# Kernel optimization log

Hardware: AMD Instinct MI355X
Metric: run time of the kernel (lower is better)

## Reference

```python
import jax, jax.numpy as jnp
import numpy as np

B, N, C, H = 8, 1024, 768, 12
TEMP = 0.1


def setup_inputs() -> dict:
    key = jax.random.key(0)
    k1, k2, k3 = jax.random.split(key, 3)
    x = jax.random.normal(k1, (B, N, C), dtype=jnp.float32)
    # nn.MultiheadAttention params (bias=False since qkv_bias=False)
    w_in = jax.random.normal(k2, (3 * C, C), dtype=jnp.float32) * 0.02   # in_proj_weight
    w_out = jax.random.normal(k3, (C, C), dtype=jnp.float32) * 0.02      # out_proj.weight
    sm_w = jnp.ones((3,), dtype=jnp.float32)                             # Conv1d(1,1,3) init ones
    return {"x": x, "w_in": w_in, "w_out": w_out, "sm_w": sm_w}


def reference(x, w_in, w_out, sm_w):
    Bq, Nq, Cq = x.shape
    hd = Cq // H
    # in-projection (torch Linear: y = x @ W^T)
    qkv = x @ w_in.T                                   # [B,N,3C]
    q, k, v = jnp.split(qkv, 3, axis=-1)
    to_heads = lambda t: t.reshape(Bq, Nq, H, hd).transpose(0, 2, 1, 3)  # [B,H,N,hd]
    q, k, v = to_heads(q), to_heads(k), to_heads(v)
    scale = 1.0 / np.sqrt(hd)
    logits = jnp.einsum("bhqd,bhkd->bhqk", q, k) * scale
    attn = jax.nn.softmax(logits, axis=-1)             # [B,H,N,N]
    ctx = jnp.einsum("bhqk,bhkd->bhqd", attn, v)
    ctx = ctx.transpose(0, 2, 1, 3).reshape(Bq, Nq, Cq)
    x_out = ctx @ w_out.T                              # [B,N,C]

    # average_attn_weights=True -> mean over heads
    aw = attn.mean(axis=1)                             # [B,N,N]
    # central finite difference with replicate padding along key dim
    p = jnp.pad(aw, ((0, 0), (0, 0), (1, 1)), mode="edge")
    grad = (p[:, :, 2:] - p[:, :, :-2]) * 0.5
    importance = jnp.abs(grad).sum(axis=1)             # sum over query dim -> [B,N]

    # Conv1d(1,1,k=3,pad=1,bias=False): cross-correlation with zero padding
    ip = jnp.pad(importance, ((0, 0), (1, 1)))
    sm = sm_w[0] * ip[:, :-2] + sm_w[1] * ip[:, 1:-1] + sm_w[2] * ip[:, 2:]

    # eval path: final_scores = importance_scores (no EMA)
    mu = sm.mean(axis=-1, keepdims=True)
    sd = jnp.std(sm, axis=-1, keepdims=True, ddof=1)   # torch std is unbiased
    fs = (sm - mu) / (sd + 1e-6)
    final_scores = jax.nn.softmax(fs / TEMP, axis=-1)  # [B,N]
    return x_out, final_scores
```

## Files before the change

### kernel.cpp

```cpp
#include <hip/hip_runtime.h>

#define NSEQ  1024
#define NHEAD 12
#define HDIM  64
#define CDIM  768
#define BATCH 8

typedef short bf16x8 __attribute__((ext_vector_type(8)));
typedef float f32x4  __attribute__((ext_vector_type(4)));

__device__ __forceinline__ float bf2f(unsigned short h) {
  unsigned u = ((unsigned)h) << 16;
  float f;
  __builtin_memcpy(&f, &u, 4);
  return f;
}
__device__ __forceinline__ unsigned short f2bf(float f) {
  unsigned u;
  __builtin_memcpy(&u, &f, 4);
  u = (u + 0x7fffu + ((u >> 16) & 1u)) >> 16;
  return (unsigned short)u;
}

__device__ __forceinline__ size_t qk_off(size_t bh, int s, int d) {
  return ((((bh * 64 + (s >> 4)) * 2 + (d >> 5)) * 64) + (((d >> 3) & 3) * 16) + (s & 15)) * 8 + (d & 7);
}
__device__ __forceinline__ size_t v_off(size_t bh, int key, int d) {
  return ((((bh * 4 + (d >> 4)) * 32 + (key >> 5)) * 64) + (((key >> 3) & 3) * 16) + (d & 15)) * 8 + (key & 7);
}

#define GLD16(GP, LP) __builtin_amdgcn_global_load_lds( \
    (const __attribute__((address_space(1))) void*)(GP), \
    (__attribute__((address_space(3))) void*)(LP), 16, 0, 0)

__global__ __launch_bounds__(256)
void convert_kernel(const float* __restrict__ x, const float* __restrict__ w_in,
                    const float* __restrict__ w_out,
                    unsigned short* __restrict__ xh, unsigned short* __restrict__ xl,
                    unsigned short* __restrict__ wih, unsigned short* __restrict__ wil,
                    unsigned short* __restrict__ woh)
{
  const int idx = (blockIdx.x * 256 + threadIdx.x) * 4;
  if (idx < 6291456) {
    float4 v = *(const float4*)(x + idx);
    ushort4 h, l;
    h.x = f2bf(v.x); l.x = f2bf(v.x - bf2f(h.x));
    h.y = f2bf(v.y); l.y = f2bf(v.y - bf2f(h.y));
    h.z = f2bf(v.z); l.z = f2bf(v.z - bf2f(h.z));
    h.w = f2bf(v.w); l.w = f2bf(v.w - bf2f(h.w));
    *(ushort4*)(xh + idx) = h;
    *(ushort4*)(xl + idx) = l;
  } else if (idx < 6291456 + 1769472) {
    const int j = idx - 6291456;
    float4 v = *(const float4*)(w_in + j);
    ushort4 h, l;
    h.x = f2bf(v.x); l.x = f2bf(v.x - bf2f(h.x));
    h.y = f2bf(v.y); l.y = f2bf(v.y - bf2f(h.y));
    h.z = f2bf(v.z); l.z = f2bf(v.z - bf2f(h.z));
    h.w = f2bf(v.w); l.w = f2bf(v.w - bf2f(h.w));
    *(ushort4*)(wih + j) = h;
    *(ushort4*)(wil + j) = l;
  } else {
    const int j = idx - 8060928;
    float4 v = *(const float4*)(w_out + j);
    ushort4 h;
    h.x = f2bf(v.x); h.y = f2bf(v.y); h.z = f2bf(v.z); h.w = f2bf(v.w);
    *(ushort4*)(woh + j) = h;
  }
}

template<int MODE>
__global__ __launch_bounds__(256)
void gemm_mfma(const unsigned short* __restrict__ Ah, const unsigned short* __restrict__ Al,
               const unsigned short* __restrict__ Bh, const unsigned short* __restrict__ Bl,
               float* __restrict__ Cout,
               unsigned short* __restrict__ Qfh, unsigned short* __restrict__ Qfl,
               unsigned short* __restrict__ Kfh, unsigned short* __restrict__ Kfl,
               unsigned short* __restrict__ Vf)
{
  __shared__ unsigned short Asm[128][64];
  __shared__ unsigned short Bsm[128][64];
  const int t    = threadIdx.x;
  const int lane = t & 63;
  const int wid  = t >> 6;
  const int c    = lane & 15;
  const int g    = lane >> 4;
  const int id   = blockIdx.x;
  const int xcd  = id & 7;
  const int j    = id >> 3;
  const int bm   = (j & 7) + xcd * 8;
  const int bn   = j >> 3;
  const int sec    = (MODE == 0) ? (bn / 6) : 0;
  const int nsteps = (MODE == 0 && sec < 2) ? 36 : 12;

  f32x4 acc[4][4];
#pragma unroll
  for (int mi = 0; mi < 4; ++mi)
#pragma unroll
    for (int ni = 0; ni < 4; ++ni) acc[mi][ni] = (f32x4){0.f, 0.f, 0.f, 0.f};

  const size_t Am0 = (size_t)bm * 128;
  const size_t Bn0 = (size_t)bn * 128;
  const int srow = wid * 32 + (lane >> 3);
  const int scol = (lane & 7) * 8;
  const int mh = (wid & 1) * 64;
  const int nh = (wid >> 1) * 64;

  for (int ks = 0; ks < nsteps; ++ks) {
    const int ksec = (ks >= 24) ? 2 : ((ks >= 12) ? 1 : 0);
    const int kin  = (ks - ksec * 12) * 64;
    const unsigned short* Asrc = (ksec == 1) ? Al : Ah;
    const unsigned short* Bsrc = (ksec == 2) ? Bl : Bh;
    __syncthreads();
#pragma unroll
    for (int i = 0; i < 4; ++i) {
      GLD16(Asrc + (Am0 + srow + i * 8) * 768 + kin + scol, &Asm[wid * 32 + i * 8][0]);
      GLD16(Bsrc + (Bn0 + srow + i * 8) * 768 + kin + scol, &Bsm[wid * 32 + i * 8][0]);
    }
    __syncthreads();
#pragma unroll
    for (int kk = 0; kk < 2; ++kk) {
      bf16x8 a[4], bb[4];
#pragma unroll
      for (int mi = 0; mi < 4; ++mi)
        a[mi] = *(const bf16x8*)&Asm[mh + mi * 16 + c][kk * 32 + g * 8];
#pragma unroll
      for (int ni = 0; ni < 4; ++ni)
        bb[ni] = *(const bf16x8*)&Bsm[nh + ni * 16 + c][kk * 32 + g * 8];
#pragma unroll
      for (int mi = 0; mi < 4; ++mi)
#pragma unroll
        for (int ni = 0; ni < 4; ++ni)
          acc[mi][ni] = __builtin_amdgcn_mfma_f32_16x16x32_bf16(a[mi], bb[ni], acc[mi][ni], 0, 0, 0);
    }
  }

  if (MODE == 1) {
#pragma unroll
    for (int mi = 0; mi < 4; ++mi) {
#pragma unroll
      for (int r = 0; r < 4; ++r) {
        const int m = bm * 128 + mh + mi * 16 + g * 4 + r;
#pragma unroll
        for (int ni = 0; ni < 4; ++ni) {
          const int n = bn * 128 + nh + ni * 16 + c;
          Cout[(size_t)m * 768 + n] = acc[mi][ni][r];
        }
      }
    }
  } else {
#pragma unroll
    for (int mi = 0; mi < 4; ++mi) {
#pragma unroll
      for (int r = 0; r < 4; ++r) {
        const int m   = bm * 128 + mh + mi * 16 + g * 4 + r;
        const int bi  = m >> 10;
        const int qi  = m & 1023;
#pragma unroll
        for (int ni = 0; ni < 4; ++ni) {
          const int n  = bn * 128 + nh + ni * 16 + c;
          const int np = n - sec * 768;
          const int h  = np >> 6;
          const int d  = np & 63;
          const size_t bh = (size_t)(bi * 12 + h);
          float v = acc[mi][ni][r];
          if (sec == 0) {
            v *= 0.125f;
            size_t off = qk_off(bh, qi, d);
            unsigned short hi = f2bf(v);
            Qfh[off] = hi;
            Qfl[off] = f2bf(v - bf2f(hi));
          } else if (sec == 1) {
            size_t off = qk_off(bh, qi, d);
            unsigned short hi = f2bf(v);
            Kfh[off] = hi;
            Kfl[off] = f2bf(v - bf2f(hi));
          } else {
            Vf[v_off(bh, qi, d)] = f2bf(v);
          }
        }
      }
    }
  }
}

struct AttnSmem {
  union {
    unsigned short P[16][1032];
    float AW[8][1032];
  } u;
  float Cpart[4][16][64];
  float red[16][4];
};

__global__ __launch_bounds__(256, 2)
void attn_mfma(const unsigned short* __restrict__ Qfh, const unsigned short* __restrict__ Qfl,
               const unsigned short* __restrict__ Kfh, const unsigned short* __restrict__ Kfl,
               const unsigned short* __restrict__ Vf,
               unsigned short* __restrict__ CtxG, float* __restrict__ Imp)
{
  __shared__ AttnSmem sm;
  const int t    = threadIdx.x;
  const int lane = t & 63;
  const int wid  = t >> 6;
  const int g    = lane >> 4;
  const int c    = lane & 15;
  const int b    = blockIdx.x & 7;
  const int qt   = blockIdx.x >> 3;
  const int q0   = qt * 16;

  float aw[16][4];
#pragma unroll
  for (int kt = 0; kt < 16; ++kt)
#pragma unroll
    for (int r = 0; r < 4; ++r) aw[kt][r] = 0.f;

  for (int h = 0; h < 12; ++h) {
    const size_t bh = (size_t)b * 12 + h;

    const size_t qbase = ((bh * 64 + qt) * 2) * 512 + lane * 8;
    bf16x8 qh0 = *(const bf16x8*)(Qfh + qbase);
    bf16x8 qh1 = *(const bf16x8*)(Qfh + qbase + 512);
    bf16x8 ql0 = *(const bf16x8*)(Qfl + qbase);
    bf16x8 ql1 = *(const bf16x8*)(Qfl + qbase + 512);

    f32x4 acc[16];
#pragma unroll
    for (int kt = 0; kt < 16; ++kt) acc[kt] = (f32x4){0.f, 0.f, 0.f, 0.f};
    const size_t kbase = ((bh * 64 + wid * 16) * 2) * 512 + lane * 8;
#pragma unroll
    for (int kt = 0; kt < 16; ++kt) {
      const size_t kb = kbase + (size_t)kt * 1024;
      bf16x8 kh0 = *(const bf16x8*)(Kfh + kb);
      bf16x8 kh1 = *(const bf16x8*)(Kfh + kb + 512);
      bf16x8 kl0 = *(const bf16x8*)(Kfl + kb);
      bf16x8 kl1 = *(const bf16x8*)(Kfl + kb + 512);
      f32x4 a = acc[kt];
      a = __builtin_amdgcn_mfma_f32_16x16x32_bf16(qh0, kh0, a, 0, 0, 0);
      a = __builtin_amdgcn_mfma_f32_16x16x32_bf16(qh1, kh1, a, 0, 0, 0);
      a = __builtin_amdgcn_mfma_f32_16x16x32_bf16(qh0, kl0, a, 0, 0, 0);
      a = __builtin_amdgcn_mfma_f32_16x16x32_bf16(qh1, kl1, a, 0, 0, 0);
      a = __builtin_amdgcn_mfma_f32_16x16x32_bf16(ql0, kh0, a, 0, 0, 0);
      a = __builtin_amdgcn_mfma_f32_16x16x32_bf16(ql1, kh1, a, 0, 0, 0);
      acc[kt] = a;
    }

    float sume[4];
#pragma unroll
    for (int r = 0; r < 4; ++r) {
      float s = 0.f;
#pragma unroll
      for (int kt = 0; kt < 16; ++kt) {
        float e = __expf(fminf(acc[kt][r], 80.f));
        acc[kt][r] = e;
        s += e;
      }
      s += __shfl_xor(s, 1);
      s += __shfl_xor(s, 2);
      s += __shfl_xor(s, 4);
      s += __shfl_xor(s, 8);
      sume[r] = s;
    }
    if (c == 0) {
#pragma unroll
      for (int r = 0; r < 4; ++r) sm.red[g * 4 + r][wid] = sume[r];
    }
    __syncthreads();
#pragma unroll
    for (int r = 0; r < 4; ++r) {
      const float* rp = sm.red[g * 4 + r];
      float inv = 1.f / ((rp[0] + rp[1]) + (rp[2] + rp[3]));
#pragma unroll
      for (int kt = 0; kt < 16; ++kt) {
        float p = acc[kt][r] * inv;
        aw[kt][r] += p * (1.f / 12.f);
        sm.u.P[g * 4 + r][wid * 256 + kt * 16 + c] = f2bf(p);
      }
    }

    f32x4 cacc[4];
#pragma unroll
    for (int dt = 0; dt < 4; ++dt) cacc[dt] = (f32x4){0.f, 0.f, 0.f, 0.f};
    const size_t vbase = (bh * 4) * 32 * 512 + (size_t)wid * 8 * 512 + lane * 8;
#pragma unroll
    for (int ks = 0; ks < 8; ++ks) {
      bf16x8 pf = *(const bf16x8*)&sm.u.P[c][wid * 256 + ks * 32 + g * 8];
#pragma unroll
      for (int dt = 0; dt < 4; ++dt) {
        bf16x8 vf = *(const bf16x8*)(Vf + vbase + ((size_t)dt * 32 + ks) * 512);
        cacc[dt] = __builtin_amdgcn_mfma_f32_16x16x32_bf16(pf, vf, cacc[dt], 0, 0, 0);
      }
    }
#pragma unroll
    for (int dt = 0; dt < 4; ++dt)
#pragma unroll
      for (int r = 0; r < 4; ++r)
        sm.Cpart[wid][g * 4 + r][dt * 16 + c] = cacc[dt][r];
    __syncthreads();
    for (int i = t; i < 1024; i += 256) {
      int qi = i >> 6, d = i & 63;
      float s = (sm.Cpart[0][qi][d] + sm.Cpart[1][qi][d]) +
                (sm.Cpart[2][qi][d] + sm.Cpart[3][qi][d]);
      CtxG[((size_t)(b * 1024 + q0 + qi)) * 768 + h * 64 + d] = f2bf(s);
    }
    __syncthreads();
  }

  float ia[4] = {0.f, 0.f, 0.f, 0.f};
#pragma unroll
  for (int half = 0; half < 2; ++half) {
    if ((g >> 1) == half) {
#pragma unroll
      for (int kt = 0; kt < 16; ++kt)
#pragma unroll
        for (int r = 0; r < 4; ++r)
          sm.u.AW[(g & 1) * 4 + r][wid * 256 + kt * 16 + c] = aw[kt][r];
    }
    __syncthreads();
#pragma unroll
    for (int qi = 0; qi < 8; ++qi) {
#pragma unroll
      for (int cc = 0; cc < 4; ++cc) {
        int k = t * 4 + cc;
        float am = sm.u.AW[qi][k == 0 ? 0 : k - 1];
        float ap = sm.u.AW[qi][k == 1023 ? 1023 : k + 1];
        ia[cc] += fabsf((ap - am) * 0.5f);
      }
    }
    __syncthreads();
  }
#pragma unroll
  for (int cc = 0; cc < 4; ++cc)
    atomicAdd(&Imp[b * 1024 + t * 4 + cc], ia[cc]);
}

__device__ inline float blk_sum(float v, volatile float* wbuf, int t) {
#pragma unroll
  for (int off = 32; off > 0; off >>= 1) v += __shfl_xor(v, off);
  __syncthreads();
  if ((t & 63) == 0) wbuf[t >> 6] = v;
  __syncthreads();
  return (wbuf[0] + wbuf[1]) + (wbuf[2] + wbuf[3]);
}
__device__ inline float blk_max(float v, volatile float* wbuf, int t) {
#pragma unroll
  for (int off = 32; off > 0; off >>= 1) v = fmaxf(v, __shfl_xor(v, off));
  __syncthreads();
  if ((t & 63) == 0) wbuf[t >> 6] = v;
  __syncthreads();
  return fmaxf(fmaxf(wbuf[0], wbuf[1]), fmaxf(wbuf[2], wbuf[3]));
}

__global__ __launch_bounds__(256)
void scores_kernel(const float* __restrict__ Imp, const float* __restrict__ smw,
                   float* __restrict__ Out)
{
  __shared__ float ip[1026];
  __shared__ float wbuf[4];
  const int b = blockIdx.x;
  const int t = threadIdx.x;

  if (t == 0) { ip[0] = 0.f; ip[1025] = 0.f; }
  float4 iv = *(const float4*)(Imp + (size_t)b * 1024 + t * 4);
  ip[1 + t * 4 + 0] = iv.x;
  ip[1 + t * 4 + 1] = iv.y;
  ip[1 + t * 4 + 2] = iv.z;
  ip[1 + t * 4 + 3] = iv.w;
  __syncthreads();

  const float w0 = smw[0], w1 = smw[1], w2 = smw[2];
  float smv[4];
#pragma unroll
  for (int j = 0; j < 4; ++j) {
    int k = t * 4 + j;
    smv[j] = w0 * ip[k] + w1 * ip[k + 1] + w2 * ip[k + 2];
  }
  float tot = blk_sum((smv[0] + smv[1]) + (smv[2] + smv[3]), wbuf, t);
  float mu  = tot * (1.f / 1024.f);
  float lv = 0.f;
#pragma unroll
  for (int j = 0; j < 4; ++j) { float d = smv[j] - mu; lv += d * d; }
  float var = blk_sum(lv, wbuf, t) * (1.f / 1023.f);
  float inv = 1.f / (sqrtf(var) + 1e-6f);
  float fs[4];
#pragma unroll
  for (int j = 0; j < 4; ++j) fs[j] = (smv[j] - mu) * inv * 10.f;
  float M = blk_max(fmaxf(fmaxf(fs[0], fs[1]), fmaxf(fs[2], fs[3])), wbuf, t);
  float e[4]; float ls = 0.f;
#pragma unroll
  for (int j = 0; j < 4; ++j) { e[j] = __expf(fs[j] - M); ls += e[j]; }
  float S = blk_sum(ls, wbuf, t);
  float r = 1.f / S;
  float4 o = {e[0] * r, e[1] * r, e[2] * r, e[3] * r};
  *(float4*)(Out + (size_t)b * 1024 + t * 4) = o;
}

extern "C" void kernel_launch(void* const* d_in, const int* in_sizes, int n_in,
                              void* d_out, int out_size, void* d_ws, size_t ws_size,
                              hipStream_t stream)
{
  const float* x     = (const float*)d_in[0];
  const float* w_in  = (const float*)d_in[1];
  const float* w_out = (const float*)d_in[2];
  const float* smw   = (const float*)d_in[3];
  float* out = (float*)d_out;

  const size_t SZx  = 6291456;
  const size_t SZw  = 1769472;
  const size_t SZwo = 589824;

  unsigned short* xh   = (unsigned short*)d_ws;
  unsigned short* xl   = xh + SZx;
  unsigned short* wih  = xl + SZx;
  unsigned short* wil  = wih + SZw;
  unsigned short* woh  = wil + SZw;
  unsigned short* qfh  = woh + SZwo;
  unsigned short* qfl  = qfh + SZx;
  unsigned short* kfh  = qfl + SZx;
  unsigned short* kfl  = kfh + SZx;
  unsigned short* vf   = kfl + SZx;
  unsigned short* ctxb = vf + SZx;
  float* imp = (float*)(ctxb + SZx);

  hipMemsetAsync(imp, 0, BATCH * NSEQ * sizeof(float), stream);

  convert_kernel<<<8448, 256, 0, stream>>>(x, w_in, w_out, xh, xl, wih, wil, woh);
  gemm_mfma<0><<<1152, 256, 0, stream>>>(xh, xl, wih, wil, nullptr,
                                         qfh, qfl, kfh, kfl, vf);
  attn_mfma<<<512, 256, 0, stream>>>(qfh, qfl, kfh, kfl, vf, ctxb, imp);
  gemm_mfma<1><<<384, 256, 0, stream>>>(ctxb, nullptr, woh, nullptr, out,
                                        nullptr, nullptr, nullptr, nullptr, nullptr);
  scores_kernel<<<8, 256, 0, stream>>>(imp, smw, out + SZx);
}
```

Before: 358.9 us.

## Split attention keys over eight waves and alias ctx partials onto P buffer

The attention kernel now runs 512-thread blocks of eight waves, each covering 128 keys instead of 256. This halves per-wave accumulator registers and adds waves to hide load latency. The per-wave context partials now reuse the P shared buffer instead of a separate Cpart array, shrinking shared memory so more blocks fit per CU. The Q/K hi-lo split and the bf16 P conversion switch to truncation instead of round-to-nearest, saving a few ALU ops at a small accuracy cost. The final cross-wave reduction now sums eight partials.

```diff
diff --git a/kernel.cpp b/kernel.cpp
--- a/kernel.cpp
+++ b/kernel.cpp
@@ -20,6 +20,11 @@
   __builtin_memcpy(&u, &f, 4);
   u = (u + 0x7fffu + ((u >> 16) & 1u)) >> 16;
   return (unsigned short)u;
+}
+__device__ __forceinline__ unsigned short f2bf_rz(float f) {
+  unsigned u;
+  __builtin_memcpy(&u, &f, 4);
+  return (unsigned short)(u >> 16);
 }
 
 __device__ __forceinline__ size_t qk_off(size_t bh, int s, int d) {
@@ -167,14 +172,14 @@
           if (sec == 0) {
             v *= 0.125f;
             size_t off = qk_off(bh, qi, d);
-            unsigned short hi = f2bf(v);
+            unsigned short hi = f2bf_rz(v);
             Qfh[off] = hi;
-            Qfl[off] = f2bf(v - bf2f(hi));
+            Qfl[off] = f2bf_rz(v - bf2f(hi));
           } else if (sec == 1) {
             size_t off = qk_off(bh, qi, d);
-            unsigned short hi = f2bf(v);
+            unsigned short hi = f2bf_rz(v);
             Kfh[off] = hi;
-            Kfl[off] = f2bf(v - bf2f(hi));
+            Kfl[off] = f2bf_rz(v - bf2f(hi));
           } else {
             Vf[v_off(bh, qi, d)] = f2bf(v);
           }
@@ -186,14 +191,13 @@
 
 struct AttnSmem {
   union {
-    unsigned short P[16][1032];
-    float AW[8][1032];
+    unsigned short Pu[16][1028];
+    float AW[8][1028];
   } u;
-  float Cpart[4][16][64];
-  float red[16][4];
+  float red[16][8];
 };
 
-__global__ __launch_bounds__(256, 2)
+__global__ __launch_bounds__(512, 4)
 void attn_mfma(const unsigned short* __restrict__ Qfh, const unsigned short* __restrict__ Qfl,
                const unsigned short* __restrict__ Kfh, const unsigned short* __restrict__ Kfl,
                const unsigned short* __restrict__ Vf,
@@ -209,9 +213,9 @@
   const int qt   = blockIdx.x >> 3;
   const int q0   = qt * 16;
 
-  float aw[16][4];
-#pragma unroll
-  for (int kt = 0; kt < 16; ++kt)
+  float aw[8][4];
+#pragma unroll
+  for (int kt = 0; kt < 8; ++kt)
 #pragma unroll
     for (int r = 0; r < 4; ++r) aw[kt][r] = 0.f;
 
@@ -224,12 +228,12 @@
     bf16x8 ql0 = *(const bf16x8*)(Qfl + qbase);
     bf16x8 ql1 = *(const bf16x8*)(Qfl + qbase + 512);
 
-    f32x4 acc[16];
-#pragma unroll
-    for (int kt = 0; kt < 16; ++kt) acc[kt] = (f32x4){0.f, 0.f, 0.f, 0.f};
-    const size_t kbase = ((bh * 64 + wid * 16) * 2) * 512 + lane * 8;
-#pragma unroll
-    for (int kt = 0; kt < 16; ++kt) {
+    f32x4 acc[8];
+#pragma unroll
+    for (int kt = 0; kt < 8; ++kt) acc[kt] = (f32x4){0.f, 0.f, 0.f, 0.f};
+    const size_t kbase = ((bh * 64 + wid * 8) * 2) * 512 + lane * 8;
+#pragma unroll
+    for (int kt = 0; kt < 8; ++kt) {
       const size_t kb = kbase + (size_t)kt * 1024;
       bf16x8 kh0 = *(const bf16x8*)(Kfh + kb);
       bf16x8 kh1 = *(const bf16x8*)(Kfh + kb + 512);
@@ -250,7 +254,7 @@
     for (int r = 0; r < 4; ++r) {
       float s = 0.f;
 #pragma unroll
-      for (int kt = 0; kt < 16; ++kt) {
+      for (int kt = 0; kt < 8; ++kt) {
         float e = __expf(fminf(acc[kt][r], 80.f));
         acc[kt][r] = e;
         s += e;
@@ -269,59 +273,65 @@
 #pragma unroll
     for (int r = 0; r < 4; ++r) {
       const float* rp = sm.red[g * 4 + r];
-      float inv = 1.f / ((rp[0] + rp[1]) + (rp[2] + rp[3]));
-#pragma unroll
-      for (int kt = 0; kt < 16; ++kt) {
+      float tot = ((rp[0] + rp[1]) + (rp[2] + rp[3])) +
+                  ((rp[4] + rp[5]) + (rp[6] + rp[7]));
+      float inv = 1.f / tot;
+#pragma unroll
+      for (int kt = 0; kt < 8; ++kt) {
         float p = acc[kt][r] * inv;
         aw[kt][r] += p * (1.f / 12.f);
-        sm.u.P[g * 4 + r][wid * 256 + kt * 16 + c] = f2bf(p);
+        sm.u.Pu[g * 4 + r][wid * 128 + kt * 16 + c] = f2bf_rz(p);
       }
     }
 
     f32x4 cacc[4];
 #pragma unroll
     for (int dt = 0; dt < 4; ++dt) cacc[dt] = (f32x4){0.f, 0.f, 0.f, 0.f};
-    const size_t vbase = (bh * 4) * 32 * 512 + (size_t)wid * 8 * 512 + lane * 8;
-#pragma unroll
-    for (int ks = 0; ks < 8; ++ks) {
-      bf16x8 pf = *(const bf16x8*)&sm.u.P[c][wid * 256 + ks * 32 + g * 8];
+#pragma unroll
+    for (int ks = 0; ks < 4; ++ks) {
+      bf16x8 pf = *(const bf16x8*)&sm.u.Pu[c][wid * 128 + ks * 32 + g * 8];
 #pragma unroll
       for (int dt = 0; dt < 4; ++dt) {
-        bf16x8 vf = *(const bf16x8*)(Vf + vbase + ((size_t)dt * 32 + ks) * 512);
+        bf16x8 vf = *(const bf16x8*)(Vf + (((size_t)(bh * 4 + dt)) * 32 + wid * 4 + ks) * 512 + lane * 8);
         cacc[dt] = __builtin_amdgcn_mfma_f32_16x16x32_bf16(pf, vf, cacc[dt], 0, 0, 0);
       }
     }
 #pragma unroll
-    for (int dt = 0; dt < 4; ++dt)
-#pragma unroll
-      for (int r = 0; r < 4; ++r)
-        sm.Cpart[wid][g * 4 + r][dt * 16 + c] = cacc[dt][r];
-    __syncthreads();
-    for (int i = t; i < 1024; i += 256) {
+    for (int dt = 0; dt < 4; ++dt) {
+#pragma unroll
+      for (int r = 0; r < 4; ++r) {
+        float* cw = (float*)&sm.u.Pu[g * 4 + r][wid * 128];
+        cw[dt * 16 + c] = cacc[dt][r];
+      }
+    }
+    __syncthreads();
+    for (int i = t; i < 1024; i += 512) {
       int qi = i >> 6, d = i & 63;
-      float s = (sm.Cpart[0][qi][d] + sm.Cpart[1][qi][d]) +
-                (sm.Cpart[2][qi][d] + sm.Cpart[3][qi][d]);
+      const float* cf = (const float*)&sm.u.Pu[qi][0];
+      float s = 0.f;
+#pragma unroll
+      for (int w = 0; w < 8; ++w) s += cf[w * 64 + d];
       CtxG[((size_t)(b * 1024 + q0 + qi)) * 768 + h * 64 + d] = f2bf(s);
     }
     __syncthreads();
   }
 
-  float ia[4] = {0.f, 0.f, 0.f, 0.f};
+  float ia[2] = {0.f, 0.f};
 #pragma unroll
   for (int half = 0; half < 2; ++half) {
     if ((g >> 1) == half) {
 #pragma unroll
-      for (int kt = 0; kt < 16; ++kt)
+      for (int kt = 0; kt < 8; ++kt)
 #pragma unroll
         for (int r = 0; r < 4; ++r)
-          sm.u.AW[(g & 1) * 4 + r][wid * 256 + kt * 16 + c] = aw[kt][r];
+          sm.u.AW[(g & 1) * 4 + r][wid * 128 + kt * 16 + c] = aw[kt][r];
     }
     __syncthreads();
 #pragma unroll
     for (int qi = 0; qi < 8; ++qi) {
 #pragma unroll
-      for (int cc = 0; cc < 4; ++cc) {
-        int k = t * 4 + cc;
+      for (int cc = 0; cc < 2; ++cc) {
+        int k = t * 2 + cc;
         float am = sm.u.AW[qi][k == 0 ? 0 : k - 1];
         float ap = sm.u.AW[qi][k == 1023 ? 1023 : k + 1];
         ia[cc] += fabsf((ap - am) * 0.5f);
@@ -330,8 +340,8 @@
     __syncthreads();
   }
 #pragma unroll
-  for (int cc = 0; cc < 4; ++cc)
-    atomicAdd(&Imp[b * 1024 + t * 4 + cc], ia[cc]);
+  for (int cc = 0; cc < 2; ++cc)
+    atomicAdd(&Imp[b * 1024 + t * 2 + cc], ia[cc]);
 }
 
 __device__ inline float blk_sum(float v, volatile float* wbuf, int t) {
@@ -427,7 +437,7 @@
   convert_kernel<<<8448, 256, 0, stream>>>(x, w_in, w_out, xh, xl, wih, wil, woh);
   gemm_mfma<0><<<1152, 256, 0, stream>>>(xh, xl, wih, wil, nullptr,
                                          qfh, qfl, kfh, kfl, vf);
-  attn_mfma<<<512, 256, 0, stream>>>(qfh, qfl, kfh, kfl, vf, ctxb, imp);
+  attn_mfma<<<512, 512, 0, stream>>>(qfh, qfl, kfh, kfl, vf, ctxb, imp);
   gemm_mfma<1><<<384, 256, 0, stream>>>(ctxb, nullptr, woh, nullptr, out,
                                         nullptr, nullptr, nullptr, nullptr, nullptr);
   scores_kernel<<<8, 256, 0, stream>>>(imp, smw, out + SZx);
```

After: 360.6 us. About the same (+0.5%).
